# Performance work log

Measured on AMD Instinct MI355X. Metric: run time of the kernel, lower is better.

## Reference

```python
import jax, jax.numpy as jnp
import numpy as np

B, T, W, H = 8, 4096, 1024, 8
BW = W // H

def setup_inputs() -> dict:
    key = jax.random.key(0)
    ks = jax.random.split(key, 6)
    x = jax.random.normal(ks[0], (B, T, W), dtype=jnp.float32)
    std = 1.0 / np.sqrt(BW)  # w_init_variance_scale=1.0
    w_in = jax.random.normal(ks[1], (H, BW, BW), dtype=jnp.float32) * std
    b_in = jnp.zeros((H, BW), dtype=jnp.float32)
    w_a = jax.random.normal(ks[2], (H, BW, BW), dtype=jnp.float32) * std
    b_a = jnp.zeros((H, BW), dtype=jnp.float32)
    # rnn_param_init: uniform on ring radius [0.9, 0.999], softplus-inverse transform
    eps = 1e-8
    u = jax.random.uniform(ks[3], (W,), minval=0.9**2 + eps, maxval=0.999**2 + eps)
    t = 0.5 * jnp.log(u)
    a_param = jnp.log(jnp.exp(-t) - 1.0).astype(jnp.float32)
    return {"x": x, "w_in": w_in, "b_in": b_in, "w_a": w_a, "b_a": b_a, "a_param": a_param}

def _bdl(x, w, b):
    # block-diagonal linear: [..., (h i)] -> [..., (h j)]
    xh = x.reshape(x.shape[:-1] + (H, BW))
    y = jnp.einsum('bthi,hij->bthj', xh, w) + b
    return y.reshape(x.shape)

def reference(x, w_in, b_in, w_a, b_a, a_param):
    gate_x = jax.nn.sigmoid(_bdl(x, w_in, b_in))
    gate_a = jax.nn.sigmoid(_bdl(x, w_a, b_a))
    log_a = -8.0 * gate_a * jax.nn.softplus(a_param)  # [B,T,W]
    a = jnp.exp(log_a)
    mult = jnp.sqrt(1.0 - jnp.exp(2.0 * log_a))
    reset = (jnp.arange(x.shape[1]) == 0)[None, :, None]  # s=None: reset at t=0
    norm_x = x * gate_x * jnp.where(reset, 1.0, mult)
    a = jnp.where(reset, 0.0, a)
    # linear recurrence h_t = a_t * h_{t-1} + norm_x_t via associative scan
    def comb(c1, c2):
        a1, h1 = c1
        a2, h2 = c2
        return (a1 * a2, a2 * h1 + h2)
    _, y = jax.lax.associative_scan(comb, (a, norm_x), axis=1)
    return y
```

## Files before the change

### kernel.cpp

```cpp
#include <hip/hip_runtime.h>

#define B_ 8
#define T_ 4096
#define W_ 1024
#define H_ 8
#define BW_ 128
#define M_ 128
#define NC_ 32
#define XS 136
#define NS_ 8

typedef __attribute__((ext_vector_type(8))) short bf16x8;
typedef __attribute__((ext_vector_type(4))) float f32x4;

__device__ __forceinline__ float bf2f(unsigned short u) {
    return __uint_as_float(((unsigned)u) << 16);
}
__device__ __forceinline__ unsigned short f2bf(float f) {
    unsigned u = __float_as_uint(f);
    u += 0x7fffu + ((u >> 16) & 1u);
    return (unsigned short)(u >> 16);
}
__device__ __forceinline__ unsigned short f2h_bits(float f) {
    union { _Float16 h; unsigned short u; } cv;
    cv.h = (_Float16)f;
    return cv.u;
}
__device__ __forceinline__ float h2f(unsigned short u) {
    union { _Float16 h; unsigned short u; } cv;
    cv.u = u;
    return (float)cv.h;
}
__device__ __forceinline__ float sigmoidf_(float z) {
    return 1.0f / (1.0f + __expf(-z));
}

__global__ __launch_bounds__(256) void prep_kernel(
    const float* __restrict__ w_in, const float* __restrict__ w_a,
    const float* __restrict__ a_param,
    unsigned short* __restrict__ wt_in, unsigned short* __restrict__ wt_a,
    float* __restrict__ cj)
{
    int gid = blockIdx.x * 256 + threadIdx.x;
    if (gid < W_) {
        float ap = a_param[gid];
        cj[gid] = -8.0f * log1pf(__expf(ap));
    }
    int mat  = gid >> 14;
    int rem  = gid & 16383;
    int hh   = rem >> 11;
    int r2   = rem & 2047;
    int seg  = r2 >> 7;
    int jrow = r2 & 127;
    const float* src = (mat ? w_a : w_in) + hh * BW_ * BW_;
    unsigned short* dst = (mat ? wt_a : wt_in) + hh * BW_ * BW_;
    unsigned short tmp[8] __attribute__((aligned(16)));
    #pragma unroll
    for (int k = 0; k < 8; ++k) tmp[k] = f2bf(src[(seg * 8 + k) * BW_ + jrow]);
    *(uint4*)(dst + jrow * BW_ + seg * 8) = *(const uint4*)tmp;
}

__global__ __launch_bounds__(1024, 8) void rg_gates(
    const float* __restrict__ x,
    const unsigned short* __restrict__ wt_in,
    const unsigned short* __restrict__ wt_a,
    const float* __restrict__ b_in,
    const float* __restrict__ b_a,
    const float* __restrict__ cj,
    float* __restrict__ aggA, float* __restrict__ aggE,
    unsigned int* __restrict__ packed)
{
    __shared__ alignas(16) unsigned short Xs[M_ * XS];
    __shared__ float2 S2[NS_ * BW_];
    __shared__ float cj_s[BW_], ba_s[BW_], bi_s[BW_];

    const int tid = threadIdx.x;
    const int bid = blockIdx.x;
    const int c = bid & (NC_ - 1);
    const int s = bid >> 5;
    const int b = s >> 3;
    const int h = s & 7;
    const int t0 = c * M_;

    const float* xg = x + ((size_t)b * T_ + t0) * W_ + h * BW_;

    #pragma unroll
    for (int r = 0; r < 4; ++r) {
        int u = tid + r * 1024;
        int t = u >> 5, sg = u & 31;
        const float4 v = *(const float4*)(xg + (size_t)t * W_ + sg * 4);
        ushort4 hv;
        hv.x = f2bf(v.x); hv.y = f2bf(v.y); hv.z = f2bf(v.z); hv.w = f2bf(v.w);
        *(ushort4*)&Xs[t * XS + sg * 4] = hv;
    }
    if (tid < BW_) {
        cj_s[tid] = cj[h * BW_ + tid];
        ba_s[tid] = b_a[h * BW_ + tid];
        bi_s[tid] = b_in[h * BW_ + tid];
    }
    __syncthreads();

    const int wave = tid >> 6;
    const int lane = tid & 63;
    const int q  = lane >> 4;
    const int cl = lane & 15;
    const int mw = wave >> 1;
    const int nw = wave & 1;

    const unsigned short* wag = wt_a  + h * BW_ * BW_;
    const unsigned short* wig = wt_in + h * BW_ * BW_;

    f32x4 zero4 = {0.0f, 0.0f, 0.0f, 0.0f};
    f32x4 acc_a[4], acc_x[4];
    #pragma unroll
    for (int nt = 0; nt < 4; ++nt) { acc_a[nt] = zero4; acc_x[nt] = zero4; }

    #pragma unroll
    for (int kk = 0; kk < 4; ++kk) {
        bf16x8 af = *(const bf16x8*)&Xs[(mw * 16 + cl) * XS + kk * 32 + q * 8];
        #pragma unroll
        for (int nt = 0; nt < 4; ++nt) {
            int j = nw * 64 + nt * 16 + cl;
            size_t wo = (size_t)j * BW_ + kk * 32 + q * 8;
            bf16x8 bfa = *(const bf16x8*)(wag + wo);
            acc_a[nt] = __builtin_amdgcn_mfma_f32_16x16x32_bf16(af, bfa, acc_a[nt], 0, 0, 0);
            bf16x8 bfi = *(const bf16x8*)(wig + wo);
            acc_x[nt] = __builtin_amdgcn_mfma_f32_16x16x32_bf16(af, bfi, acc_x[nt], 0, 0, 0);
        }
    }

    unsigned int* pgc = packed + (((size_t)s * NC_ + c) * M_) * BW_;
    #pragma unroll
    for (int nt = 0; nt < 4; ++nt) {
        int j = nw * 64 + nt * 16 + cl;
        float cjv = cj_s[j], bav = ba_s[j], biv = bi_s[j];
        float A4 = 1.0f, E4 = 0.0f;
        #pragma unroll
        for (int r = 0; r < 4; ++r) {
            int tl = mw * 16 + q * 4 + r;
            float la = cjv * sigmoidf_(acc_a[nt][r] + bav);
            float a  = __expf(la);
            float gx = sigmoidf_(acc_x[nt][r] + biv);
            float xv = bf2f(Xs[tl * XS + j]);
            float mult = sqrtf(fmaxf(1.0f - a * a, 0.0f));
            if (t0 + tl == 0) { a = 0.0f; mult = 1.0f; }
            float nxv = xv * gx * mult;
            unsigned short nxb = f2h_bits(nxv);
            float nxr = h2f(nxb);
            E4 = fmaf(a, E4, nxr);
            A4 *= a;
            pgc[(size_t)tl * BW_ + j] = ((unsigned int)f2h_bits(a) << 16) | (unsigned int)nxb;
        }
        float Ap = __shfl_xor(A4, 16);
        float Ep = __shfl_xor(E4, 16);
        float E8 = ((lane >> 4) & 1) ? fmaf(A4, Ep, E4) : fmaf(Ap, E4, Ep);
        float A8 = A4 * Ap;
        Ap = __shfl_xor(A8, 32);
        Ep = __shfl_xor(E8, 32);
        float E16 = ((lane >> 5) & 1) ? fmaf(A8, Ep, E8) : fmaf(Ap, E8, Ep);
        float A16 = A8 * Ap;
        if ((lane >> 4) == 0) S2[mw * BW_ + j] = make_float2(A16, E16);
    }
    __syncthreads();

    if (tid < BW_) {
        float At = 1.0f, Et = 0.0f;
        #pragma unroll
        for (int s8 = 0; s8 < NS_; ++s8) {
            float2 v = S2[s8 * BW_ + tid];
            Et = fmaf(v.x, Et, v.y);
            At *= v.x;
        }
        size_t idx = ((size_t)s * NC_ + c) * BW_ + tid;
        aggA[idx] = At;
        aggE[idx] = Et;
    }
}

__global__ __launch_bounds__(1024, 8) void rg_scan(
    const unsigned int* __restrict__ packed,
    const float* __restrict__ aggA, const float* __restrict__ aggE,
    float* __restrict__ y)
{
    __shared__ float2 S2[NS_ * BW_];
    __shared__ float qin[NS_ * BW_];

    const int tid = threadIdx.x;
    const int bid = blockIdx.x;
    const int c = bid & (NC_ - 1);
    const int s = bid >> 5;
    const int b = s >> 3;
    const int h = s & 7;

    const unsigned int* pg = packed + (((size_t)s * NC_ + c) * M_) * BW_;
    const int j  = tid & 127;
    const int qq = tid >> 7;

    unsigned int v[16];
    #pragma unroll
    for (int i = 0; i < 16; ++i)
        v[i] = pg[(size_t)(qq * 16 + i) * BW_ + j];

    float A = 1.0f, E = 0.0f;
    #pragma unroll
    for (int i = 0; i < 16; ++i) {
        float a  = h2f((unsigned short)(v[i] >> 16));
        float nx = h2f((unsigned short)(v[i] & 0xffffu));
        E = fmaf(a, E, nx);
        A *= a;
    }
    S2[qq * BW_ + j] = make_float2(A, E);
    __syncthreads();

    if (tid < BW_) {
        const float* pA = aggA + ((size_t)s * NC_) * BW_ + tid;
        const float* pE = aggE + ((size_t)s * NC_) * BW_ + tid;
        float hh = 0.0f;
        for (int cc = 0; cc < c; ++cc)
            hh = fmaf(pA[(size_t)cc * BW_], hh, pE[(size_t)cc * BW_]);
        #pragma unroll
        for (int s8 = 0; s8 < NS_; ++s8) {
            qin[s8 * BW_ + tid] = hh;
            float2 w = S2[s8 * BW_ + tid];
            hh = fmaf(w.x, hh, w.y);
        }
    }
    __syncthreads();

    float hcur = qin[qq * BW_ + j];
    float* yg = y + ((size_t)b * T_ + c * M_) * W_ + h * BW_ + j;
    #pragma unroll
    for (int i = 0; i < 16; ++i) {
        float a  = h2f((unsigned short)(v[i] >> 16));
        float nx = h2f((unsigned short)(v[i] & 0xffffu));
        hcur = fmaf(a, hcur, nx);
        yg[(size_t)(qq * 16 + i) * W_] = hcur;
    }
}

extern "C" void kernel_launch(void* const* d_in, const int* in_sizes, int n_in,
                              void* d_out, int out_size, void* d_ws, size_t ws_size,
                              hipStream_t stream)
{
    const float* x     = (const float*)d_in[0];
    const float* w_in  = (const float*)d_in[1];
    const float* b_in  = (const float*)d_in[2];
    const float* w_a   = (const float*)d_in[3];
    const float* b_a   = (const float*)d_in[4];
    const float* a_par = (const float*)d_in[5];
    float* y = (float*)d_out;

    char* ws = (char*)d_ws;
    unsigned short* wt_in = (unsigned short*)(ws);
    unsigned short* wt_a  = (unsigned short*)(ws + 262144);
    float* cj    = (float*)(ws + 524288);
    float* aggA  = (float*)(ws + 528384);
    float* aggE  = (float*)(ws + 1576960);
    unsigned int* packed = (unsigned int*)(ws + 2625536);

    const size_t NEED = 2625536ull + (size_t)B_ * T_ * W_ * 4ull;
    if (ws_size < NEED) return;

    prep_kernel<<<dim3(128), dim3(256), 0, stream>>>(w_in, w_a, a_par, wt_in, wt_a, cj);
    rg_gates<<<dim3(2048), dim3(1024), 0, stream>>>(
        x, wt_in, wt_a, b_in, b_a, cj, aggA, aggE, packed);
    rg_scan<<<dim3(2048), dim3(1024), 0, stream>>>(packed, aggA, aggE, y);
}
```

Before: 422.9 us.

## Halve block size, keep weight fragments in registers, vectorize scan to two channels per thread

The gates kernel now runs with 512 threads. Each of its 8 waves owns 16 output columns, so the B (weight) fragments are loaded once into registers and reused across all 8 row tiles. Before, every wave reloaded weights from global memory for each tile. The scan kernel also moves to 512 threads, with each thread handling two adjacent channels through uint2 loads and float2 stores, which widens the memory transactions. The trade-offs are more registers per thread (16 accumulators), the same MFMA count spread over fewer waves, and lower thread-level parallelism per block.

```diff
diff --git a/kernel.cpp b/kernel.cpp
--- a/kernel.cpp
+++ b/kernel.cpp
@@ -60,7 +60,7 @@
     *(uint4*)(dst + jrow * BW_ + seg * 8) = *(const uint4*)tmp;
 }
 
-__global__ __launch_bounds__(1024, 8) void rg_gates(
+__global__ __launch_bounds__(512, 4) void rg_gates(
     const float* __restrict__ x,
     const unsigned short* __restrict__ wt_in,
     const unsigned short* __restrict__ wt_a,
@@ -82,11 +82,26 @@
     const int h = s & 7;
     const int t0 = c * M_;
 
+    const int wave = tid >> 6;
+    const int lane = tid & 63;
+    const int q  = lane >> 4;
+    const int cl = lane & 15;
+    const int j  = wave * 16 + cl;
+
+    const unsigned short* wag = wt_a  + h * BW_ * BW_;
+    const unsigned short* wig = wt_in + h * BW_ * BW_;
+    bf16x8 bwa[4], bwi[4];
+    #pragma unroll
+    for (int kk = 0; kk < 4; ++kk) {
+        size_t wo = (size_t)j * BW_ + kk * 32 + q * 8;
+        bwa[kk] = *(const bf16x8*)(wag + wo);
+        bwi[kk] = *(const bf16x8*)(wig + wo);
+    }
+
     const float* xg = x + ((size_t)b * T_ + t0) * W_ + h * BW_;
-
-    #pragma unroll
-    for (int r = 0; r < 4; ++r) {
-        int u = tid + r * 1024;
+    #pragma unroll
+    for (int r = 0; r < 8; ++r) {
+        int u = tid + r * 512;
         int t = u >> 5, sg = u & 31;
         const float4 v = *(const float4*)(xg + (size_t)t * W_ + sg * 4);
         ushort4 hv;
@@ -100,47 +115,32 @@
     }
     __syncthreads();
 
-    const int wave = tid >> 6;
-    const int lane = tid & 63;
-    const int q  = lane >> 4;
-    const int cl = lane & 15;
-    const int mw = wave >> 1;
-    const int nw = wave & 1;
-
-    const unsigned short* wag = wt_a  + h * BW_ * BW_;
-    const unsigned short* wig = wt_in + h * BW_ * BW_;
-
     f32x4 zero4 = {0.0f, 0.0f, 0.0f, 0.0f};
-    f32x4 acc_a[4], acc_x[4];
-    #pragma unroll
-    for (int nt = 0; nt < 4; ++nt) { acc_a[nt] = zero4; acc_x[nt] = zero4; }
+    f32x4 acc_a[8], acc_x[8];
+    #pragma unroll
+    for (int rt = 0; rt < 8; ++rt) { acc_a[rt] = zero4; acc_x[rt] = zero4; }
 
     #pragma unroll
     for (int kk = 0; kk < 4; ++kk) {
-        bf16x8 af = *(const bf16x8*)&Xs[(mw * 16 + cl) * XS + kk * 32 + q * 8];
-        #pragma unroll
-        for (int nt = 0; nt < 4; ++nt) {
-            int j = nw * 64 + nt * 16 + cl;
-            size_t wo = (size_t)j * BW_ + kk * 32 + q * 8;
-            bf16x8 bfa = *(const bf16x8*)(wag + wo);
-            acc_a[nt] = __builtin_amdgcn_mfma_f32_16x16x32_bf16(af, bfa, acc_a[nt], 0, 0, 0);
-            bf16x8 bfi = *(const bf16x8*)(wig + wo);
-            acc_x[nt] = __builtin_amdgcn_mfma_f32_16x16x32_bf16(af, bfi, acc_x[nt], 0, 0, 0);
-        }
-    }
-
-    unsigned int* pgc = packed + (((size_t)s * NC_ + c) * M_) * BW_;
-    #pragma unroll
-    for (int nt = 0; nt < 4; ++nt) {
-        int j = nw * 64 + nt * 16 + cl;
-        float cjv = cj_s[j], bav = ba_s[j], biv = bi_s[j];
+        #pragma unroll
+        for (int rt = 0; rt < 8; ++rt) {
+            bf16x8 af = *(const bf16x8*)&Xs[(rt * 16 + cl) * XS + kk * 32 + q * 8];
+            acc_a[rt] = __builtin_amdgcn_mfma_f32_16x16x32_bf16(af, bwa[kk], acc_a[rt], 0, 0, 0);
+            acc_x[rt] = __builtin_amdgcn_mfma_f32_16x16x32_bf16(af, bwi[kk], acc_x[rt], 0, 0, 0);
+        }
+    }
+
+    unsigned int* pgc = packed + ((size_t)(s * NC_ + c) * M_) * BW_;
+    const float cjv = cj_s[j], bav = ba_s[j], biv = bi_s[j];
+    #pragma unroll
+    for (int rt = 0; rt < 8; ++rt) {
         float A4 = 1.0f, E4 = 0.0f;
         #pragma unroll
         for (int r = 0; r < 4; ++r) {
-            int tl = mw * 16 + q * 4 + r;
-            float la = cjv * sigmoidf_(acc_a[nt][r] + bav);
+            int tl = rt * 16 + q * 4 + r;
+            float la = cjv * sigmoidf_(acc_a[rt][r] + bav);
             float a  = __expf(la);
-            float gx = sigmoidf_(acc_x[nt][r] + biv);
+            float gx = sigmoidf_(acc_x[rt][r] + biv);
             float xv = bf2f(Xs[tl * XS + j]);
             float mult = sqrtf(fmaxf(1.0f - a * a, 0.0f));
             if (t0 + tl == 0) { a = 0.0f; mult = 1.0f; }
@@ -159,7 +159,7 @@
         Ep = __shfl_xor(E8, 32);
         float E16 = ((lane >> 5) & 1) ? fmaf(A8, Ep, E8) : fmaf(Ap, E8, Ep);
         float A16 = A8 * Ap;
-        if ((lane >> 4) == 0) S2[mw * BW_ + j] = make_float2(A16, E16);
+        if ((lane >> 4) == 0) S2[rt * BW_ + j] = make_float2(A16, E16);
     }
     __syncthreads();
 
@@ -177,7 +177,7 @@
     }
 }
 
-__global__ __launch_bounds__(1024, 8) void rg_scan(
+__global__ __launch_bounds__(512, 4) void rg_scan(
     const unsigned int* __restrict__ packed,
     const float* __restrict__ aggA, const float* __restrict__ aggE,
     float* __restrict__ y)
@@ -192,49 +192,65 @@
     const int b = s >> 3;
     const int h = s & 7;
 
-    const unsigned int* pg = packed + (((size_t)s * NC_ + c) * M_) * BW_;
-    const int j  = tid & 127;
-    const int qq = tid >> 7;
-
-    unsigned int v[16];
+    const uint2* pg = (const uint2*)(packed + ((size_t)(s * NC_ + c) * M_) * BW_);
+    const int j2 = tid & 63;
+    const int qq = tid >> 6;
+    const int jb = j2 * 2;
+
+    uint2 v[16];
     #pragma unroll
     for (int i = 0; i < 16; ++i)
-        v[i] = pg[(size_t)(qq * 16 + i) * BW_ + j];
-
-    float A = 1.0f, E = 0.0f;
+        v[i] = pg[(size_t)(qq * 16 + i) * 64 + j2];
+
+    float A0 = 1.0f, E0 = 0.0f, A1 = 1.0f, E1 = 0.0f;
     #pragma unroll
     for (int i = 0; i < 16; ++i) {
-        float a  = h2f((unsigned short)(v[i] >> 16));
-        float nx = h2f((unsigned short)(v[i] & 0xffffu));
-        E = fmaf(a, E, nx);
-        A *= a;
-    }
-    S2[qq * BW_ + j] = make_float2(A, E);
-    __syncthreads();
-
-    if (tid < BW_) {
-        const float* pA = aggA + ((size_t)s * NC_) * BW_ + tid;
-        const float* pE = aggE + ((size_t)s * NC_) * BW_ + tid;
-        float hh = 0.0f;
-        for (int cc = 0; cc < c; ++cc)
-            hh = fmaf(pA[(size_t)cc * BW_], hh, pE[(size_t)cc * BW_]);
+        float a0  = h2f((unsigned short)(v[i].x >> 16));
+        float n0  = h2f((unsigned short)(v[i].x & 0xffffu));
+        float a1  = h2f((unsigned short)(v[i].y >> 16));
+        float n1  = h2f((unsigned short)(v[i].y & 0xffffu));
+        E0 = fmaf(a0, E0, n0);  A0 *= a0;
+        E1 = fmaf(a1, E1, n1);  A1 *= a1;
+    }
+    S2[qq * BW_ + jb]     = make_float2(A0, E0);
+    S2[qq * BW_ + jb + 1] = make_float2(A1, E1);
+    __syncthreads();
+
+    if (tid < 64) {
+        const float* pA = aggA + (size_t)s * NC_ * BW_;
+        const float* pE = aggE + (size_t)s * NC_ * BW_;
+        float h0 = 0.0f, h1 = 0.0f;
+        for (int cc = 0; cc < c; ++cc) {
+            const float2 a2 = *(const float2*)(pA + (size_t)cc * BW_ + tid * 2);
+            const float2 e2 = *(const float2*)(pE + (size_t)cc * BW_ + tid * 2);
+            h0 = fmaf(a2.x, h0, e2.x);
+            h1 = fmaf(a2.y, h1, e2.y);
+        }
         #pragma unroll
         for (int s8 = 0; s8 < NS_; ++s8) {
-            qin[s8 * BW_ + tid] = hh;
-            float2 w = S2[s8 * BW_ + tid];
-            hh = fmaf(w.x, hh, w.y);
-        }
-    }
-    __syncthreads();
-
-    float hcur = qin[qq * BW_ + j];
-    float* yg = y + ((size_t)b * T_ + c * M_) * W_ + h * BW_ + j;
+            qin[s8 * BW_ + tid * 2]     = h0;
+            qin[s8 * BW_ + tid * 2 + 1] = h1;
+            float2 g0 = S2[s8 * BW_ + tid * 2];
+            float2 g1 = S2[s8 * BW_ + tid * 2 + 1];
+            h0 = fmaf(g0.x, h0, g0.y);
+            h1 = fmaf(g1.x, h1, g1.y);
+        }
+    }
+    __syncthreads();
+
+    float h0 = qin[qq * BW_ + jb];
+    float h1 = qin[qq * BW_ + jb + 1];
+    float* yg = y + ((size_t)b * T_ + c * M_) * W_ + h * BW_ + jb;
     #pragma unroll
     for (int i = 0; i < 16; ++i) {
-        float a  = h2f((unsigned short)(v[i] >> 16));
-        float nx = h2f((unsigned short)(v[i] & 0xffffu));
-        hcur = fmaf(a, hcur, nx);
-        yg[(size_t)(qq * 16 + i) * W_] = hcur;
+        float a0  = h2f((unsigned short)(v[i].x >> 16));
+        float n0  = h2f((unsigned short)(v[i].x & 0xffffu));
+        float a1  = h2f((unsigned short)(v[i].y >> 16));
+        float n1  = h2f((unsigned short)(v[i].y & 0xffffu));
+        h0 = fmaf(a0, h0, n0);
+        h1 = fmaf(a1, h1, n1);
+        float2 out = make_float2(h0, h1);
+        *(float2*)(yg + (size_t)(qq * 16 + i) * W_) = out;
     }
 }
 
@@ -262,7 +278,7 @@
     if (ws_size < NEED) return;
 
     prep_kernel<<<dim3(128), dim3(256), 0, stream>>>(w_in, w_a, a_par, wt_in, wt_a, cj);
-    rg_gates<<<dim3(2048), dim3(1024), 0, stream>>>(
+    rg_gates<<<dim3(2048), dim3(512), 0, stream>>>(
         x, wt_in, wt_a, b_in, b_a, cj, aggA, aggE, packed);
-    rg_scan<<<dim3(2048), dim3(1024), 0, stream>>>(packed, aggA, aggE, y);
-}
+    rg_scan<<<dim3(2048), dim3(512), 0, stream>>>(packed, aggA, aggE, y);
+}
```

After: 339.3 us. -19.8%, faster.
